# Optimization experiments

Hardware: AMD Instinct MI355X
Metric: run time of the kernel (lower is better)

## Reference

```python
import jax, jax.numpy as jnp
import numpy as np

RNN_SIZE = 1024
TSTEPS = 256
BATCH = 128


def setup_inputs() -> dict:
    key = jax.random.key(0)
    k1, k2, k3, k4, k5 = jax.random.split(key, 5)
    H = RNN_SIZE
    scale = 1.0 / np.sqrt(H)
    return {
        "cell_inputs": jax.random.normal(k1, (BATCH, H), dtype=jnp.float32),
        "hidden_states": jax.random.normal(k2, (BATCH, H), dtype=jnp.float32),
        # Keras GRUCell params (reset_after=True, default):
        "kernel": jax.random.normal(k3, (H, 3 * H), dtype=jnp.float32) * scale,
        "recurrent_kernel": jax.random.normal(k4, (H, 3 * H), dtype=jnp.float32) * scale,
        "bias": jax.random.normal(k5, (2, 3 * H), dtype=jnp.float32) * 0.01,
    }


def _gru_step(x, h, kernel, recurrent_kernel, bias):
    # Keras GRUCell math with reset_after=True (TF2 default).
    b_in, b_rec = bias[0], bias[1]
    mx = x @ kernel + b_in            # [B, 3H]
    mh = h @ recurrent_kernel + b_rec  # [B, 3H]
    xz, xr, xh = jnp.split(mx, 3, axis=-1)
    hz, hr, hh = jnp.split(mh, 3, axis=-1)
    z = jax.nn.sigmoid(xz + hz)
    r = jax.nn.sigmoid(xr + hr)
    h_cand = jnp.tanh(xh + r * hh)
    h_new = z * h + (1.0 - z) * h_cand
    return h_new  # GRUCell output == new state


def reference(cell_inputs, hidden_states, kernel, recurrent_kernel, bias):
    def step(carry, _):
        x, h = carry
        h_new = _gru_step(x, h, kernel, recurrent_kernel, bias)
        return (h_new, h_new), h_new

    (x_f, h_f), outs = jax.lax.scan(step, (cell_inputs, hidden_states), None, length=TSTEPS)
    outputs = jnp.transpose(outs, (1, 0, 2))  # [B, T, H]
    return outputs, h_f
```

## Files before the change

### kernel.cpp

```cpp
#include <hip/hip_runtime.h>
#include <hip/hip_bf16.h>

#define H 1024
#define B3H 3072
#define BATCH 128
#define TSTEPS 256
#define LROW 520
#define PLANE (16 * LROW)

typedef __attribute__((ext_vector_type(8))) short short8;
typedef __attribute__((ext_vector_type(4))) float f32x4;

static __device__ __forceinline__ float bf2f(__hip_bfloat16 v) { return __bfloat162float(v); }
static __device__ __forceinline__ unsigned short f2bf_bits(float f) {
    __hip_bfloat16 h = __float2bfloat16(f);
    return __builtin_bit_cast(unsigned short, h);
}
static __device__ __forceinline__ float bits2f(unsigned short b) {
    return bf2f(__builtin_bit_cast(__hip_bfloat16, b));
}
static __device__ __forceinline__ unsigned short bfbits(__hip_bfloat16 v) {
    return __builtin_bit_cast(unsigned short, v);
}
static __device__ __forceinline__ void split_bf(float v, unsigned short& hi, unsigned short& lo) {
    hi = f2bf_bits(v);
    lo = f2bf_bits(v - bits2f(hi));
}

#define PW_OFF   256
#define PWL_OFF  (PW_OFF + 12582912)
#define XHI_OFF  (PWL_OFF + 12582912)
#define XLO_OFF  (XHI_OFF + 262144)
#define H0HI_OFF (XLO_OFF + 262144)
#define H0LO_OFF (H0HI_OFF + 262144)
#define H1HI_OFF (H0LO_OFF + 262144)
#define H1LO_OFF (H1HI_OFF + 262144)

__global__ void detect_dtype(const unsigned int* __restrict__ w, int* __restrict__ flag) {
    __shared__ int cnt[256];
    int c = 0;
    for (int i = threadIdx.x; i < 4096; i += 256) {
        unsigned int v = (w[i] >> 8) & 0x7f;
        c += (v >= 0x33 && v <= 0x3f) ? 1 : 0;
    }
    cnt[threadIdx.x] = c;
    __syncthreads();
    for (int s = 128; s > 0; s >>= 1) {
        if (threadIdx.x < s) cnt[threadIdx.x] += cnt[threadIdx.x + s];
        __syncthreads();
    }
    if (threadIdx.x == 0) *flag = (cnt[0] * 2 > 4096) ? 1 : 0;
}

__global__ void pack_w(const void* __restrict__ Kp, const void* __restrict__ Rp,
                       __hip_bfloat16* __restrict__ pwh, __hip_bfloat16* __restrict__ pwl,
                       const int* __restrict__ flag) {
    int idx = blockIdx.x * 256 + threadIdx.x;
    int lane = idx & 63;
    int kc   = (idx >> 6) & 31;
    int ns   = (idx >> 11) & 1;
    int it   = (idx >> 12) & 31;
    int g    = idx >> 17;
    if (g >= 6) return;
    const int isbf = *flag;
    int col   = (g % 3) * 1024 + it * 32 + ns * 16 + (lane & 15);
    int kbase = kc * 32 + (lane >> 4) * 8;
    unsigned short eh[8], el[8];
    if (isbf) {
        const __hip_bfloat16* src = (const __hip_bfloat16*)((g < 3) ? Kp : Rp);
#pragma unroll
        for (int j = 0; j < 8; ++j) { eh[j] = bfbits(src[(size_t)(kbase + j) * B3H + col]); el[j] = 0; }
    } else {
        const float* src = (const float*)((g < 3) ? Kp : Rp);
#pragma unroll
        for (int j = 0; j < 8; ++j) split_bf(src[(size_t)(kbase + j) * B3H + col], eh[j], el[j]);
    }
    uint4 vh, vl;
    vh.x = (unsigned int)eh[0] | ((unsigned int)eh[1] << 16);
    vh.y = (unsigned int)eh[2] | ((unsigned int)eh[3] << 16);
    vh.z = (unsigned int)eh[4] | ((unsigned int)eh[5] << 16);
    vh.w = (unsigned int)eh[6] | ((unsigned int)eh[7] << 16);
    vl.x = (unsigned int)el[0] | ((unsigned int)el[1] << 16);
    vl.y = (unsigned int)el[2] | ((unsigned int)el[3] << 16);
    vl.z = (unsigned int)el[4] | ((unsigned int)el[5] << 16);
    vl.w = (unsigned int)el[6] | ((unsigned int)el[7] << 16);
    *(uint4*)(pwh + (size_t)idx * 8) = vh;
    *(uint4*)(pwl + (size_t)idx * 8) = vl;
}

__global__ void init_bufs(const void* __restrict__ cin, const void* __restrict__ hs,
                          unsigned short* __restrict__ xhi, unsigned short* __restrict__ xlo,
                          unsigned short* __restrict__ hhi, unsigned short* __restrict__ hlo,
                          const int* __restrict__ flag) {
    int i = blockIdx.x * 256 + threadIdx.x;
    if (i >= BATCH * H) return;
    float xv, hv;
    if (*flag) {
        xv = bf2f(((const __hip_bfloat16*)cin)[i]);
        hv = bf2f(((const __hip_bfloat16*)hs)[i]);
    } else {
        xv = ((const float*)cin)[i];
        hv = ((const float*)hs)[i];
    }
    unsigned short a, b;
    split_bf(xv, a, b); xhi[i] = a; xlo[i] = b;
    split_bf(hv, a, b); hhi[i] = a; hlo[i] = b;
}

__launch_bounds__(384)
__global__ void gru_step(const unsigned short* __restrict__ aAhi,
                         const unsigned short* __restrict__ aAlo,
                         const unsigned short* __restrict__ aBhi,
                         const unsigned short* __restrict__ aBlo,
                         unsigned short* __restrict__ dsthi,
                         unsigned short* __restrict__ dstlo,
                         const __hip_bfloat16* __restrict__ pwh,
                         const __hip_bfloat16* __restrict__ pwl,
                         const void* __restrict__ bias,
                         void* __restrict__ out,
                         const int* __restrict__ flag,
                         int t, int same_xh, int write_hf) {
    __shared__ unsigned short sA[4 * PLANE];

    const int tid  = threadIdx.x;
    const int g    = tid >> 6;
    const int lane = tid & 63;
    const int bt = blockIdx.x >> 5;
    const int it = blockIdx.x & 31;
    const int bbase = bt * 16;
    const int m0 = lane & 15;
    const int q  = lane >> 4;

    const size_t boff0 = ((size_t)((g * 32 + it) * 2 + 0) * 32) * 64 + lane;
    const size_t boff1 = ((size_t)((g * 32 + it) * 2 + 1) * 32) * 64 + lane;
    const uint4* bh0 = (const uint4*)pwh + boff0;
    const uint4* bh1 = (const uint4*)pwh + boff1;
    const uint4* bl0 = (const uint4*)pwl + boff0;
    const uint4* bl1 = (const uint4*)pwl + boff1;

    const unsigned short* aH = sA + (((g < 3) || same_xh) ? 0 : 2) * PLANE;
    const unsigned short* aL = aH + PLANE;

    f32x4 acc0 = {0.f, 0.f, 0.f, 0.f};
    f32x4 acc1 = {0.f, 0.f, 0.f, 0.f};

    const int nplanes = same_xh ? 2 : 4;
    const int nGr = nplanes * 1024;

    for (int c = 0; c < 2; ++c) {
        if (c) __syncthreads();
        const int kstart = c * 512;
        for (int g4 = tid; g4 < nGr; g4 += 384) {
            int plane = g4 >> 10;
            int rem   = g4 & 1023;
            int row   = rem >> 6;
            int kg    = rem & 63;
            const unsigned short* src =
                (plane == 0) ? aAhi : (plane == 1) ? aAlo : (plane == 2) ? aBhi : aBlo;
            uint4 v = *(const uint4*)&src[(size_t)(bbase + row) * H + kstart + kg * 8];
            *(uint4*)&sA[plane * PLANE + row * LROW + kg * 8] = v;
        }
        __syncthreads();
#pragma unroll 4
        for (int kc = 0; kc < 16; ++kc) {
            const int kcg = c * 16 + kc;
            short8 b0h = __builtin_bit_cast(short8, bh0[(size_t)kcg * 64]);
            short8 b1h = __builtin_bit_cast(short8, bh1[(size_t)kcg * 64]);
            short8 b0l = __builtin_bit_cast(short8, bl0[(size_t)kcg * 64]);
            short8 b1l = __builtin_bit_cast(short8, bl1[(size_t)kcg * 64]);
            const int koff = kc * 32 + q * 8;
            short8 a_h = *(const short8*)&aH[m0 * LROW + koff];
            short8 a_l = *(const short8*)&aL[m0 * LROW + koff];
            acc0 = __builtin_amdgcn_mfma_f32_16x16x32_bf16(a_h, b0h, acc0, 0, 0, 0);
            acc1 = __builtin_amdgcn_mfma_f32_16x16x32_bf16(a_h, b1h, acc1, 0, 0, 0);
            acc0 = __builtin_amdgcn_mfma_f32_16x16x32_bf16(a_h, b0l, acc0, 0, 0, 0);
            acc1 = __builtin_amdgcn_mfma_f32_16x16x32_bf16(a_h, b1l, acc1, 0, 0, 0);
            acc0 = __builtin_amdgcn_mfma_f32_16x16x32_bf16(a_l, b0h, acc0, 0, 0, 0);
            acc1 = __builtin_amdgcn_mfma_f32_16x16x32_bf16(a_l, b1h, acc1, 0, 0, 0);
        }
    }

    __syncthreads();
    float* sG = (float*)sA;
    {
#pragma unroll
        for (int r = 0; r < 4; ++r) {
            int mrow = q * 4 + r;
            sG[g * 512 + mrow * 32 + m0]      = acc0[r];
            sG[g * 512 + mrow * 32 + m0 + 16] = acc1[r];
        }
    }
    __syncthreads();

    const int isbf = *flag;
    const __hip_bfloat16* bias_b = (const __hip_bfloat16*)bias;
    const float* bias_f = (const float*)bias;
    __hip_bfloat16* outb = (__hip_bfloat16*)out;
    float* outf = (float*)out;

    const int ibase0 = it * 32;
    for (int e = tid; e < 512; e += 384) {
        int mloc = e >> 5;
        int nloc = e & 31;
        int b = bbase + mloc;
        int i = ibase0 + nloc;
        float xz = sG[0 * 512 + e], xr = sG[1 * 512 + e], xh = sG[2 * 512 + e];
        float hz = sG[3 * 512 + e], hr = sG[4 * 512 + e], hh = sG[5 * 512 + e];
        float bi0 = isbf ? bf2f(bias_b[i])              : bias_f[i];
        float bi1 = isbf ? bf2f(bias_b[1024 + i])       : bias_f[1024 + i];
        float bi2 = isbf ? bf2f(bias_b[2048 + i])       : bias_f[2048 + i];
        float br0 = isbf ? bf2f(bias_b[B3H + i])        : bias_f[B3H + i];
        float br1 = isbf ? bf2f(bias_b[B3H + 1024 + i]) : bias_f[B3H + 1024 + i];
        float br2 = isbf ? bf2f(bias_b[B3H + 2048 + i]) : bias_f[B3H + 2048 + i];
        float zlin = xz + bi0 + hz + br0;
        float rlin = xr + bi1 + hr + br1;
        float xht  = xh + bi2;
        float hht  = hh + br2;
        float z  = 1.0f / (1.0f + expf(-zlin));
        float r  = 1.0f / (1.0f + expf(-rlin));
        float hc = tanhf(xht + r * hht);
        size_t hidx = (size_t)b * H + i;
        float hold = bits2f(aBhi[hidx]) + bits2f(aBlo[hidx]);
        float hnew = z * hold + (1.0f - z) * hc;
        unsigned short nh, nl;
        split_bf(hnew, nh, nl);
        dsthi[hidx] = nh;
        dstlo[hidx] = nl;
        size_t o1 = (size_t)b * (TSTEPS * H) + (size_t)t * H + i;
        size_t o2 = (size_t)BATCH * TSTEPS * H + hidx;
        if (isbf) {
            outb[o1] = __float2bfloat16(hnew);
            if (write_hf) outb[o2] = __float2bfloat16(hnew);
        } else {
            outf[o1] = hnew;
            if (write_hf) outf[o2] = hnew;
        }
    }
}

extern "C" void kernel_launch(void* const* d_in, const int* in_sizes, int n_in,
                              void* d_out, int out_size, void* d_ws, size_t ws_size,
                              hipStream_t stream) {
    const void* cin  = d_in[0];
    const void* hs   = d_in[1];
    const void* Kw   = d_in[2];
    const void* Rw   = d_in[3];
    const void* bias = d_in[4];

    char* ws = (char*)d_ws;
    int* flag = (int*)ws;
    __hip_bfloat16* pwh = (__hip_bfloat16*)(ws + PW_OFF);
    __hip_bfloat16* pwl = (__hip_bfloat16*)(ws + PWL_OFF);
    unsigned short* xhi  = (unsigned short*)(ws + XHI_OFF);
    unsigned short* xlo  = (unsigned short*)(ws + XLO_OFF);
    unsigned short* hhi[2] = {(unsigned short*)(ws + H0HI_OFF), (unsigned short*)(ws + H1HI_OFF)};
    unsigned short* hlo[2] = {(unsigned short*)(ws + H0LO_OFF), (unsigned short*)(ws + H1LO_OFF)};

    detect_dtype<<<1, 256, 0, stream>>>((const unsigned int*)Kw, flag);
    pack_w<<<3072, 256, 0, stream>>>(Kw, Rw, pwh, pwl, flag);
    init_bufs<<<512, 256, 0, stream>>>(cin, hs, xhi, xlo, hhi[0], hlo[0], flag);

    for (int t = 0; t < TSTEPS; ++t) {
        int cur = t & 1, nxt = (t + 1) & 1;
        const unsigned short* Ahi = (t == 0) ? xhi : hhi[cur];
        const unsigned short* Alo = (t == 0) ? xlo : hlo[cur];
        gru_step<<<256, 384, 0, stream>>>(Ahi, Alo, hhi[cur], hlo[cur],
                                          hhi[nxt], hlo[nxt], pwh, pwl, bias,
                                          (void*)d_out, flag,
                                          t, (t == 0) ? 0 : 1, (t == TSTEPS - 1) ? 1 : 0);
    }
}
```

Before: 4.570 ms.

## Fuse all GRU timesteps into one persistent cooperative kernel with grid sync

Replaces 256 per-timestep kernel launches with a single cooperative launch of 256 blocks that loops over time and uses grid.sync() between steps. Bias values are cached in shared memory once, and the previous hidden state for each block's own outputs is kept in shared memory, so it no longer has to be re-read from global memory. This removes launch overhead and inter-kernel gaps, but each step now pays for a grid-wide barrier and the kernel needs every block to be co-resident.

```diff
diff --git a/kernel.cpp b/kernel.cpp
--- a/kernel.cpp
+++ b/kernel.cpp
@@ -1,5 +1,6 @@
 #include <hip/hip_runtime.h>
 #include <hip/hip_bf16.h>
+#include <hip/hip_cooperative_groups.h>
 
 #define H 1024
 #define B3H 3072
@@ -107,20 +108,23 @@
     split_bf(hv, a, b); hhi[i] = a; hlo[i] = b;
 }
 
-__launch_bounds__(384)
-__global__ void gru_step(const unsigned short* __restrict__ aAhi,
-                         const unsigned short* __restrict__ aAlo,
-                         const unsigned short* __restrict__ aBhi,
-                         const unsigned short* __restrict__ aBlo,
-                         unsigned short* __restrict__ dsthi,
-                         unsigned short* __restrict__ dstlo,
-                         const __hip_bfloat16* __restrict__ pwh,
-                         const __hip_bfloat16* __restrict__ pwl,
-                         const void* __restrict__ bias,
-                         void* __restrict__ out,
-                         const int* __restrict__ flag,
-                         int t, int same_xh, int write_hf) {
+__launch_bounds__(384, 1)
+__global__ void gru_persistent(const unsigned short* __restrict__ xhi,
+                               const unsigned short* __restrict__ xlo,
+                               unsigned short* __restrict__ h0hi,
+                               unsigned short* __restrict__ h0lo,
+                               unsigned short* __restrict__ h1hi,
+                               unsigned short* __restrict__ h1lo,
+                               const __hip_bfloat16* __restrict__ pwh,
+                               const __hip_bfloat16* __restrict__ pwl,
+                               const void* __restrict__ bias,
+                               void* __restrict__ out,
+                               const int* __restrict__ flag) {
+    cooperative_groups::grid_group grid = cooperative_groups::this_grid();
+
     __shared__ unsigned short sA[4 * PLANE];
+    __shared__ float sHold[512];
+    __shared__ float sBias[192];
 
     const int tid  = threadIdx.x;
     const int g    = tid >> 6;
@@ -130,6 +134,19 @@
     const int bbase = bt * 16;
     const int m0 = lane & 15;
     const int q  = lane >> 4;
+    const int ibase0 = it * 32;
+    const int isbf = *flag;
+
+    {
+        const __hip_bfloat16* bias_b = (const __hip_bfloat16*)bias;
+        const float* bias_f = (const float*)bias;
+        for (int e = tid; e < 192; e += 384) {
+            int gg = e >> 5;
+            int i  = ibase0 + (e & 31);
+            int src = (gg < 3) ? (gg * 1024 + i) : (B3H + (gg - 3) * 1024 + i);
+            sBias[e] = isbf ? bf2f(bias_b[src]) : bias_f[src];
+        }
+    }
 
     const size_t boff0 = ((size_t)((g * 32 + it) * 2 + 0) * 32) * 64 + lane;
     const size_t boff1 = ((size_t)((g * 32 + it) * 2 + 1) * 32) * 64 + lane;
@@ -138,103 +155,104 @@
     const uint4* bl0 = (const uint4*)pwl + boff0;
     const uint4* bl1 = (const uint4*)pwl + boff1;
 
-    const unsigned short* aH = sA + (((g < 3) || same_xh) ? 0 : 2) * PLANE;
-    const unsigned short* aL = aH + PLANE;
-
-    f32x4 acc0 = {0.f, 0.f, 0.f, 0.f};
-    f32x4 acc1 = {0.f, 0.f, 0.f, 0.f};
-
-    const int nplanes = same_xh ? 2 : 4;
-    const int nGr = nplanes * 1024;
-
-    for (int c = 0; c < 2; ++c) {
-        if (c) __syncthreads();
-        const int kstart = c * 512;
-        for (int g4 = tid; g4 < nGr; g4 += 384) {
-            int plane = g4 >> 10;
-            int rem   = g4 & 1023;
-            int row   = rem >> 6;
-            int kg    = rem & 63;
-            const unsigned short* src =
-                (plane == 0) ? aAhi : (plane == 1) ? aAlo : (plane == 2) ? aBhi : aBlo;
-            uint4 v = *(const uint4*)&src[(size_t)(bbase + row) * H + kstart + kg * 8];
-            *(uint4*)&sA[plane * PLANE + row * LROW + kg * 8] = v;
-        }
-        __syncthreads();
-#pragma unroll 4
-        for (int kc = 0; kc < 16; ++kc) {
-            const int kcg = c * 16 + kc;
-            short8 b0h = __builtin_bit_cast(short8, bh0[(size_t)kcg * 64]);
-            short8 b1h = __builtin_bit_cast(short8, bh1[(size_t)kcg * 64]);
-            short8 b0l = __builtin_bit_cast(short8, bl0[(size_t)kcg * 64]);
-            short8 b1l = __builtin_bit_cast(short8, bl1[(size_t)kcg * 64]);
-            const int koff = kc * 32 + q * 8;
-            short8 a_h = *(const short8*)&aH[m0 * LROW + koff];
-            short8 a_l = *(const short8*)&aL[m0 * LROW + koff];
-            acc0 = __builtin_amdgcn_mfma_f32_16x16x32_bf16(a_h, b0h, acc0, 0, 0, 0);
-            acc1 = __builtin_amdgcn_mfma_f32_16x16x32_bf16(a_h, b1h, acc1, 0, 0, 0);
-            acc0 = __builtin_amdgcn_mfma_f32_16x16x32_bf16(a_h, b0l, acc0, 0, 0, 0);
-            acc1 = __builtin_amdgcn_mfma_f32_16x16x32_bf16(a_h, b1l, acc1, 0, 0, 0);
-            acc0 = __builtin_amdgcn_mfma_f32_16x16x32_bf16(a_l, b0h, acc0, 0, 0, 0);
-            acc1 = __builtin_amdgcn_mfma_f32_16x16x32_bf16(a_l, b1h, acc1, 0, 0, 0);
-        }
-    }
-
-    __syncthreads();
-    float* sG = (float*)sA;
-    {
-#pragma unroll
-        for (int r = 0; r < 4; ++r) {
-            int mrow = q * 4 + r;
-            sG[g * 512 + mrow * 32 + m0]      = acc0[r];
-            sG[g * 512 + mrow * 32 + m0 + 16] = acc1[r];
-        }
-    }
-    __syncthreads();
-
-    const int isbf = *flag;
-    const __hip_bfloat16* bias_b = (const __hip_bfloat16*)bias;
-    const float* bias_f = (const float*)bias;
     __hip_bfloat16* outb = (__hip_bfloat16*)out;
     float* outf = (float*)out;
 
-    const int ibase0 = it * 32;
-    for (int e = tid; e < 512; e += 384) {
-        int mloc = e >> 5;
-        int nloc = e & 31;
-        int b = bbase + mloc;
-        int i = ibase0 + nloc;
-        float xz = sG[0 * 512 + e], xr = sG[1 * 512 + e], xh = sG[2 * 512 + e];
-        float hz = sG[3 * 512 + e], hr = sG[4 * 512 + e], hh = sG[5 * 512 + e];
-        float bi0 = isbf ? bf2f(bias_b[i])              : bias_f[i];
-        float bi1 = isbf ? bf2f(bias_b[1024 + i])       : bias_f[1024 + i];
-        float bi2 = isbf ? bf2f(bias_b[2048 + i])       : bias_f[2048 + i];
-        float br0 = isbf ? bf2f(bias_b[B3H + i])        : bias_f[B3H + i];
-        float br1 = isbf ? bf2f(bias_b[B3H + 1024 + i]) : bias_f[B3H + 1024 + i];
-        float br2 = isbf ? bf2f(bias_b[B3H + 2048 + i]) : bias_f[B3H + 2048 + i];
-        float zlin = xz + bi0 + hz + br0;
-        float rlin = xr + bi1 + hr + br1;
-        float xht  = xh + bi2;
-        float hht  = hh + br2;
-        float z  = 1.0f / (1.0f + expf(-zlin));
-        float r  = 1.0f / (1.0f + expf(-rlin));
-        float hc = tanhf(xht + r * hht);
-        size_t hidx = (size_t)b * H + i;
-        float hold = bits2f(aBhi[hidx]) + bits2f(aBlo[hidx]);
-        float hnew = z * hold + (1.0f - z) * hc;
-        unsigned short nh, nl;
-        split_bf(hnew, nh, nl);
-        dsthi[hidx] = nh;
-        dstlo[hidx] = nl;
-        size_t o1 = (size_t)b * (TSTEPS * H) + (size_t)t * H + i;
-        size_t o2 = (size_t)BATCH * TSTEPS * H + hidx;
-        if (isbf) {
-            outb[o1] = __float2bfloat16(hnew);
-            if (write_hf) outb[o2] = __float2bfloat16(hnew);
-        } else {
-            outf[o1] = hnew;
-            if (write_hf) outf[o2] = hnew;
-        }
+    for (int t = 0; t < TSTEPS; ++t) {
+        const int cur = t & 1;
+        const unsigned short* curhi = cur ? h1hi : h0hi;
+        const unsigned short* curlo = cur ? h1lo : h0lo;
+        unsigned short* dsthi = cur ? h0hi : h1hi;
+        unsigned short* dstlo = cur ? h0lo : h1lo;
+        const unsigned short* aAhi = t ? curhi : xhi;
+        const unsigned short* aAlo = t ? curlo : xlo;
+        const int same_xh = (t != 0);
+        const unsigned short* aH = sA + (((g < 3) || same_xh) ? 0 : 2) * PLANE;
+        const unsigned short* aL = aH + PLANE;
+        const int nGr = (same_xh ? 2 : 4) * 1024;
+
+        f32x4 acc0 = {0.f, 0.f, 0.f, 0.f};
+        f32x4 acc1 = {0.f, 0.f, 0.f, 0.f};
+
+        for (int c = 0; c < 2; ++c) {
+            if (c) __syncthreads();
+            const int kstart = c * 512;
+            for (int g4 = tid; g4 < nGr; g4 += 384) {
+                int plane = g4 >> 10;
+                int rem   = g4 & 1023;
+                int row   = rem >> 6;
+                int kg    = rem & 63;
+                const unsigned short* src =
+                    (plane == 0) ? aAhi : (plane == 1) ? aAlo : (plane == 2) ? curhi : curlo;
+                uint4 v = *(const uint4*)&src[(size_t)(bbase + row) * H + kstart + kg * 8];
+                *(uint4*)&sA[plane * PLANE + row * LROW + kg * 8] = v;
+            }
+            __syncthreads();
+#pragma unroll 4
+            for (int kc = 0; kc < 16; ++kc) {
+                const int kcg = c * 16 + kc;
+                short8 b0h = __builtin_bit_cast(short8, bh0[(size_t)kcg * 64]);
+                short8 b1h = __builtin_bit_cast(short8, bh1[(size_t)kcg * 64]);
+                short8 b0l = __builtin_bit_cast(short8, bl0[(size_t)kcg * 64]);
+                short8 b1l = __builtin_bit_cast(short8, bl1[(size_t)kcg * 64]);
+                const int koff = kc * 32 + q * 8;
+                short8 a_h = *(const short8*)&aH[m0 * LROW + koff];
+                short8 a_l = *(const short8*)&aL[m0 * LROW + koff];
+                acc0 = __builtin_amdgcn_mfma_f32_16x16x32_bf16(a_h, b0h, acc0, 0, 0, 0);
+                acc1 = __builtin_amdgcn_mfma_f32_16x16x32_bf16(a_h, b1h, acc1, 0, 0, 0);
+                acc0 = __builtin_amdgcn_mfma_f32_16x16x32_bf16(a_h, b0l, acc0, 0, 0, 0);
+                acc1 = __builtin_amdgcn_mfma_f32_16x16x32_bf16(a_h, b1l, acc1, 0, 0, 0);
+                acc0 = __builtin_amdgcn_mfma_f32_16x16x32_bf16(a_l, b0h, acc0, 0, 0, 0);
+                acc1 = __builtin_amdgcn_mfma_f32_16x16x32_bf16(a_l, b1h, acc1, 0, 0, 0);
+            }
+        }
+
+        __syncthreads();
+        float* sG = (float*)sA;
+        {
+#pragma unroll
+            for (int r = 0; r < 4; ++r) {
+                int mrow = q * 4 + r;
+                sG[g * 512 + mrow * 32 + m0]      = acc0[r];
+                sG[g * 512 + mrow * 32 + m0 + 16] = acc1[r];
+            }
+        }
+        __syncthreads();
+
+        for (int e = tid; e < 512; e += 384) {
+            int mloc = e >> 5;
+            int nloc = e & 31;
+            int b = bbase + mloc;
+            int i = ibase0 + nloc;
+            float xz = sG[e], xr = sG[512 + e], xh = sG[1024 + e];
+            float hz = sG[1536 + e], hr = sG[2048 + e], hh = sG[2560 + e];
+            float zlin = xz + sBias[nloc]      + hz + sBias[96 + nloc];
+            float rlin = xr + sBias[32 + nloc] + hr + sBias[128 + nloc];
+            float xht  = xh + sBias[64 + nloc];
+            float hht  = hh + sBias[160 + nloc];
+            float z  = 1.0f / (1.0f + expf(-zlin));
+            float r  = 1.0f / (1.0f + expf(-rlin));
+            float hc = tanhf(xht + r * hht);
+            size_t hidx = (size_t)b * H + i;
+            float hold = same_xh ? sHold[e]
+                                 : (bits2f(curhi[hidx]) + bits2f(curlo[hidx]));
+            float hnew = z * hold + (1.0f - z) * hc;
+            sHold[e] = hnew;
+            unsigned short nh, nl;
+            split_bf(hnew, nh, nl);
+            dsthi[hidx] = nh;
+            dstlo[hidx] = nl;
+            size_t o1 = (size_t)b * (TSTEPS * H) + (size_t)t * H + i;
+            if (isbf) {
+                outb[o1] = __float2bfloat16(hnew);
+                if (t == TSTEPS - 1) outb[(size_t)BATCH * TSTEPS * H + hidx] = __float2bfloat16(hnew);
+            } else {
+                outf[o1] = hnew;
+                if (t == TSTEPS - 1) outf[(size_t)BATCH * TSTEPS * H + hidx] = hnew;
+            }
+        }
+
+        grid.sync();
     }
 }
 
@@ -253,20 +271,26 @@
     __hip_bfloat16* pwl = (__hip_bfloat16*)(ws + PWL_OFF);
     unsigned short* xhi  = (unsigned short*)(ws + XHI_OFF);
     unsigned short* xlo  = (unsigned short*)(ws + XLO_OFF);
-    unsigned short* hhi[2] = {(unsigned short*)(ws + H0HI_OFF), (unsigned short*)(ws + H1HI_OFF)};
-    unsigned short* hlo[2] = {(unsigned short*)(ws + H0LO_OFF), (unsigned short*)(ws + H1LO_OFF)};
+    unsigned short* h0hi = (unsigned short*)(ws + H0HI_OFF);
+    unsigned short* h0lo = (unsigned short*)(ws + H0LO_OFF);
+    unsigned short* h1hi = (unsigned short*)(ws + H1HI_OFF);
+    unsigned short* h1lo = (unsigned short*)(ws + H1LO_OFF);
 
     detect_dtype<<<1, 256, 0, stream>>>((const unsigned int*)Kw, flag);
     pack_w<<<3072, 256, 0, stream>>>(Kw, Rw, pwh, pwl, flag);
-    init_bufs<<<512, 256, 0, stream>>>(cin, hs, xhi, xlo, hhi[0], hlo[0], flag);
-
-    for (int t = 0; t < TSTEPS; ++t) {
-        int cur = t & 1, nxt = (t + 1) & 1;
-        const unsigned short* Ahi = (t == 0) ? xhi : hhi[cur];
-        const unsigned short* Alo = (t == 0) ? xlo : hlo[cur];
-        gru_step<<<256, 384, 0, stream>>>(Ahi, Alo, hhi[cur], hlo[cur],
-                                          hhi[nxt], hlo[nxt], pwh, pwl, bias,
-                                          (void*)d_out, flag,
-                                          t, (t == 0) ? 0 : 1, (t == TSTEPS - 1) ? 1 : 0);
-    }
-}
+    init_bufs<<<512, 256, 0, stream>>>(cin, hs, xhi, xlo, h0hi, h0lo, flag);
+
+    const unsigned short* xhi_c = xhi;
+    const unsigned short* xlo_c = xlo;
+    const __hip_bfloat16* pwh_c = pwh;
+    const __hip_bfloat16* pwl_c = pwl;
+    const int* flag_c = flag;
+    void* kargs[] = {
+        (void*)&xhi_c, (void*)&xlo_c,
+        (void*)&h0hi, (void*)&h0lo, (void*)&h1hi, (void*)&h1lo,
+        (void*)&pwh_c, (void*)&pwl_c,
+        (void*)&bias, (void*)&d_out, (void*)&flag_c
+    };
+    hipLaunchCooperativeKernel((void*)gru_persistent, dim3(256), dim3(384),
+                               kargs, 0, stream);
+}
```

After: 11.47 ms. 151% more time.
